# Kernel tuning notes

Measured on AMD Instinct MI355X. Metric: run time of the kernel, lower is better.

Reference implementation:

```python
import jax, jax.numpy as jnp
import numpy as np
from jax import lax

DN = ('NDHWC', 'DHWIO', 'NDHWC')
SHAPE = (33, 33, 33)
B = 2
N = 40000
C = 64


def setup_inputs() -> dict:
    key = jax.random.key(0)
    ks = jax.random.split(key, 24)
    D, H, W = SHAPE
    # unique active voxel coords (batch, z, y, x)
    rng = np.random.default_rng(0)
    idx = rng.choice(B * D * H * W, size=N, replace=False)
    b = idx // (D * H * W)
    r = idx % (D * H * W)
    coors = np.stack([b, r // (H * W), (r // W) % H, r % W], axis=1).astype(np.int32)

    def w(k, shape, scale=0.1):
        return jax.random.normal(k, shape, jnp.float32) * scale

    inp = {
        'features': jax.random.normal(ks[0], (N, 3), jnp.float32),
        'coors': jnp.asarray(coors),
        'batch_size': B,
        'w1': w(ks[1], (3, 3, 3, 3, C), 0.2), 'b1': w(ks[2], (C,), 0.05),
        'w2': w(ks[3], (3, 3, 3, C, C), 0.05), 'b2': w(ks[4], (C,), 0.05),
        'w3': w(ks[5], (3, 3, 3, C, C), 0.05), 'b3': w(ks[6], (C,), 0.05),
        'wt': w(ks[7], (3, 3, 3, C, C), 0.05), 'bt': w(ks[8], (C,), 0.05),
        'w5': w(ks[9], (3, 3, 3, C, C), 0.05), 'b5': w(ks[10], (C,), 0.05),
    }
    # folded eval-mode BatchNorm: y = x*s + h  (s = gamma/sqrt(var+eps), h = beta - mean*s)
    for i, (sk, hk) in enumerate(zip(ks[11:16], ks[16:21]), start=1):
        inp[f's{i}'] = 1.0 + 0.1 * jax.random.normal(sk, (C,), jnp.float32)
        inp[f'h{i}'] = 0.05 * jax.random.normal(hk, (C,), jnp.float32)
    return inp


def _forward(features, coors, batch_size,
             w1, b1, w2, b2, w3, b3, wt, bt, w5, b5,
             s1, h1, s2, h2, s3, h3, s4, h4, s5, h5):
    D, H, W = SHAPE
    bi, zi, yi, xi = coors[:, 0], coors[:, 1], coors[:, 2], coors[:, 3]
    # densify SparseConvTensor (zeros at inactive sites) + active mask
    x = jnp.zeros((batch_size, D, H, W, features.shape[-1]), features.dtype)
    x = x.at[bi, zi, yi, xi].set(features)
    m = jnp.zeros((batch_size, D, H, W, 1), jnp.float32).at[bi, zi, yi, xi].set(1.0)
    ones3 = jnp.ones((3, 3, 3, 1, 1), jnp.float32)

    conv = lambda a, k, pad: lax.conv_general_dilated(a, k, (1, 1, 1), pad, dimension_numbers=DN)
    # masked BN(eval) + ReLU: applied only on active sites, background stays exactly 0
    act = lambda y, mm, s, h: jnp.where(mm, jax.nn.relu(y * s + h), 0.0)

    # SparseConv3d(3,64,3): valid conv; output actives = 1-dilation of input actives
    x = conv(x, w1, 'VALID')
    m1 = conv(m, ones3, 'VALID') > 0  # [B,31,31,31,1]
    x = act(x + b1, m1, s1, h1)

    # two SubMConv3d(64,64,3) sharing indice_key: same active set, SAME padding
    x = act(conv(x, w2, 'SAME') + b2, m1, s2, h2)
    x = act(conv(x, w3, 'SAME') + b3, m1, s3, h3)

    # SparseConvTranspose3d(64,64,3,2): out = (D-1)*2+3; actives = transposed dilation
    x = lax.conv_transpose(x, wt, (2, 2, 2), 'VALID', dimension_numbers=DN)
    mT = lax.conv_transpose(m1.astype(jnp.float32), ones3, (2, 2, 2), 'VALID', dimension_numbers=DN) > 0
    x = act(x + bt, mT, s4, h4)

    # ToDense -> dense Conv3d(64,64,3) -> BN -> ReLU (dense: applied everywhere)
    x = conv(x, w5, 'VALID') + b5
    x = jax.nn.relu(x * s5 + h5)
    return jnp.transpose(x, (0, 4, 1, 2, 3))  # NCDHW like spconv ToDense output


def reference(features, coors, batch_size,
              w1, b1, w2, b2, w3, b3, wt, bt, w5, b5,
              s1, h1, s2, h2, s3, h3, s4, h4, s5, h5):
    return _forward(features, coors, batch_size,
                    w1, b1, w2, b2, w3, b3, wt, bt, w5, b5,
                    s1, h1, s2, h2, s3, h3, s4, h4, s5, h5)
```

## Files before the change

kernel.cpp:

```cpp
#include <hip/hip_runtime.h>
#include <cstdint>

constexpr int BB = 2, C = 64;
constexpr int D1 = 31;
constexpr int DP = 33;
constexpr int D4 = 63;
constexpr int D5 = 61;
constexpr int D5CUBE = D5*D5*D5;

constexpr int NV1 = BB*D1*D1*D1;
constexpr int NVP = BB*DP*DP*DP;
constexpr int NV4 = BB*D4*D4*D4;
constexpr int NV5 = BB*D5*D5*D5;

constexpr size_t alup(size_t x) { return (x + 255) & ~(size_t)255; }
constexpr size_t OB_X0  = 0;
constexpr size_t OB_M0  = alup(OB_X0  + (size_t)NVP*3*4);
constexpr size_t OB_M1P = alup(OB_M0  + (size_t)NVP*4);
constexpr size_t OB_X1  = alup(OB_M1P + (size_t)NVP*4);
constexpr size_t OB_X2  = alup(OB_X1  + (size_t)NVP*64*2);
constexpr size_t OB_X3  = alup(OB_X2  + (size_t)NVP*64*2);
constexpr size_t OB_MT  = alup(OB_X3  + (size_t)NVP*64*2);
constexpr size_t OB_X4  = alup(OB_MT  + (size_t)NV4*4);
constexpr size_t OB_WB2 = alup(OB_X4  + (size_t)NV4*64*2);
constexpr size_t OB_WB3 = alup(OB_WB2 + (size_t)27*64*64*2);
constexpr size_t OB_WBT = alup(OB_WB3 + (size_t)27*64*64*2);
constexpr size_t OB_WB5 = alup(OB_WBT + (size_t)27*64*64*2);

typedef __attribute__((ext_vector_type(8))) short short8;
typedef __attribute__((ext_vector_type(4))) float f32x4;

__device__ inline unsigned short f2bf(float f) {
  unsigned int u = __float_as_uint(f);
  u = (u + 0x7FFFu + ((u >> 16) & 1u)) >> 16;
  return (unsigned short)u;
}

template<int DD>
__device__ inline void decodev(int vox, int& b, int& z, int& y, int& x) {
  x = vox % DD; int r = vox / DD;
  y = r % DD;   r /= DD;
  z = r % DD;   b = r / DD;
}

__device__ inline int xcd_swz(int bid, int nb) {
  int q = nb >> 3, r = nb & 7;
  int xcd = bid & 7, idx = bid >> 3;
  return (xcd < r ? xcd*(q+1) : r*(q+1) + (xcd - r)*q) + idx;
}

__global__ void __launch_bounds__(256)
k_zero(float* __restrict__ x0, float* __restrict__ m0, float* __restrict__ m1p,
       unsigned short* __restrict__ x1, unsigned short* __restrict__ x2,
       unsigned short* __restrict__ x3) {
  int v = blockIdx.x*256 + threadIdx.x;
  if (v >= NVP) return;
  m0[v] = 0.f; m1p[v] = 0.f;
  x0[3*v+0] = 0.f; x0[3*v+1] = 0.f; x0[3*v+2] = 0.f;
  int x = v % DP, r = v / DP;
  int y = r % DP; r /= DP;
  int z = r % DP;
  if (x==0 || x==DP-1 || y==0 || y==DP-1 || z==0 || z==DP-1) {
    ulonglong2 zz = {0ull, 0ull};
    ulonglong2* p1 = (ulonglong2*)(x1 + (size_t)v*64);
    ulonglong2* p2 = (ulonglong2*)(x2 + (size_t)v*64);
    ulonglong2* p3 = (ulonglong2*)(x3 + (size_t)v*64);
    #pragma unroll
    for (int i = 0; i < 8; i++) { p1[i] = zz; p2[i] = zz; p3[i] = zz; }
  }
}

__global__ void k_scatter(const float* __restrict__ feat, const int* __restrict__ coors,
                          int n, float* __restrict__ x0, float* __restrict__ m0) {
  int i = blockIdx.x*blockDim.x + threadIdx.x;
  if (i >= n) return;
  int b = coors[4*i+0], z = coors[4*i+1], y = coors[4*i+2], x = coors[4*i+3];
  int v = ((b*DP + z)*DP + y)*DP + x;
  x0[v*3+0] = feat[3*i+0];
  x0[v*3+1] = feat[3*i+1];
  x0[v*3+2] = feat[3*i+2];
  m0[v] = 1.0f;
}

__global__ void __launch_bounds__(256)
k_conv1(const float* __restrict__ x0, const float* __restrict__ m0,
        unsigned short* __restrict__ x1, float* __restrict__ m1p,
        const float* __restrict__ w1, const float* __restrict__ b1,
        const float* __restrict__ s1, const float* __restrict__ h1) {
  long long t = (long long)blockIdx.x*blockDim.x + threadIdx.x;
  if (t >= (long long)NV1*C) return;
  int co  = (int)(t & 63);
  int vox = (int)(t >> 6);
  int b, z, y, x; decodev<D1>(vox, b, z, y, x);
  float sum = 0.f, mm = 0.f;
  #pragma unroll
  for (int kz=0; kz<3; kz++)
  #pragma unroll
  for (int ky=0; ky<3; ky++)
  #pragma unroll
  for (int kx=0; kx<3; kx++) {
    int iv = ((b*DP + z+kz)*DP + y+ky)*DP + (x+kx);
    mm += m0[iv];
    const float* px = x0 + iv*3;
    const float* pw = w1 + ((kz*3+ky)*3+kx)*3*64 + co;
    sum += px[0]*pw[0] + px[1]*pw[64] + px[2]*pw[128];
  }
  bool m = mm > 0.f;
  float o = m ? fmaxf((sum + b1[co])*s1[co] + h1[co], 0.f) : 0.f;
  size_t pOff = (size_t)(((b*DP + z+1)*DP + y+1)*DP + (x+1));
  x1[pOff*C + co] = f2bf(o);
  if (co == 0) m1p[pOff] = m ? 1.f : 0.f;
}

__global__ void k_repack4(const float* __restrict__ wa, const float* __restrict__ wb,
                          const float* __restrict__ wc, const float* __restrict__ wd,
                          unsigned short* __restrict__ da, unsigned short* __restrict__ db,
                          unsigned short* __restrict__ dc, unsigned short* __restrict__ dd) {
  int which = blockIdx.x / 432;
  int i = (blockIdx.x - which*432)*256 + threadIdx.x;
  const float* w = which == 0 ? wa : which == 1 ? wb : which == 2 ? wc : wd;
  unsigned short* dst = which == 0 ? da : which == 1 ? db : which == 2 ? dc : dd;
  int co = i & 63, k = (i >> 6) & 63, t = i >> 12;
  int kk = k >> 5, q = (k >> 3) & 3, j = k & 7, cb = co >> 4, l = q*16 + (co & 15);
  dst[(size_t)((t*2+kk)*4+cb)*512 + l*8 + j] = f2bf(w[i]);
}

template<int NA, int DOUT, int DIN>
__global__ void __launch_bounds__(256)
k_conv_mfma(const unsigned short* __restrict__ inBF, const unsigned short* __restrict__ wB,
            unsigned short* __restrict__ outPtr, const float* __restrict__ m1p,
            const float* __restrict__ bias, const float* __restrict__ s,
            const float* __restrict__ h) {
  constexpr int NVOX = BB*DOUT*DOUT*DOUT;
  const int lane = threadIdx.x & 63;
  const int wid  = threadIdx.x >> 6;
  const int wave = xcd_swz(blockIdx.x, gridDim.x)*4 + wid;
  const int vb   = wave * (NA*16);

  int rowb[NA];
  #pragma unroll
  for (int a = 0; a < NA; a++) {
    int vox = vb + a*16 + (lane & 15);
    vox = vox < NVOX ? vox : NVOX-1;
    int b, z, y, x; decodev<DOUT>(vox, b, z, y, x);
    rowb[a] = (((b*DIN + z)*DIN + y)*DIN + x)*64;
  }
  const int koff = (lane >> 4) * 8;

  f32x4 acc[NA][4];
  #pragma unroll
  for (int a = 0; a < NA; a++)
    #pragma unroll
    for (int cb = 0; cb < 4; cb++)
      acc[a][cb] = f32x4{0.f, 0.f, 0.f, 0.f};

  #pragma unroll 1
  for (int t = 0; t < 27; ++t) {
    int kz = t / 9, rr = t - kz*9;
    int ky = rr / 3, kx = rr - ky*3;
    const int toff = ((kz*DIN + ky)*DIN + kx)*64;
    #pragma unroll
    for (int kk = 0; kk < 2; ++kk) {
      short8 A[NA];
      #pragma unroll
      for (int a = 0; a < NA; a++)
        A[a] = *reinterpret_cast<const short8*>(inBF + rowb[a] + toff + kk*32 + koff);
      short8 Bv[4];
      const unsigned short* wp = wB + (size_t)(t*2+kk)*2048 + lane*8;
      #pragma unroll
      for (int cb = 0; cb < 4; cb++)
        Bv[cb] = *reinterpret_cast<const short8*>(wp + cb*512);
      #pragma unroll
      for (int a = 0; a < NA; a++)
        #pragma unroll
        for (int cb = 0; cb < 4; cb++)
          acc[a][cb] = __builtin_amdgcn_mfma_f32_16x16x32_bf16(A[a], Bv[cb], acc[a][cb], 0, 0, 0);
    }
  }

  float bv[4], sv[4], hv[4];
  #pragma unroll
  for (int cb = 0; cb < 4; cb++) {
    int c = cb*16 + (lane & 15);
    bv[cb] = bias[c]; sv[cb] = s[c]; hv[cb] = h[c];
  }

  #pragma unroll
  for (int a = 0; a < NA; a++)
    #pragma unroll
    for (int r = 0; r < 4; r++) {
      int vox = vb + a*16 + (lane >> 4)*4 + r;
      if (vox >= NVOX) continue;
      int b, z, y, x; decodev<DOUT>(vox, b, z, y, x);
      size_t pOff = (size_t)(((b*DP + z+1)*DP + y+1)*DP + (x+1));
      bool m = m1p[pOff] > 0.f;
      #pragma unroll
      for (int cb = 0; cb < 4; cb++) {
        float o = m ? fmaxf((acc[a][cb][r] + bv[cb])*sv[cb] + hv[cb], 0.f) : 0.f;
        outPtr[pOff*64 + cb*16 + (lane & 15)] = f2bf(o);
      }
    }
}

__global__ void __launch_bounds__(256)
k_maskT(const float* __restrict__ m1p, float* __restrict__ mt) {
  int vox = blockIdx.x*256 + threadIdx.x;
  if (vox >= NV4) return;
  int b, zo, yo, xo; decodev<D4>(vox, b, zo, yo, xo);
  float mm = 0.f;
  for (int kz = 0; kz < 3; kz++) {
    if ((zo + kz) & 1) continue;
    int izp = ((zo + kz - 2) >> 1) + 1;
    for (int ky = 0; ky < 3; ky++) {
      if ((yo + ky) & 1) continue;
      int iyp = ((yo + ky - 2) >> 1) + 1;
      for (int kx = 0; kx < 3; kx++) {
        if ((xo + kx) & 1) continue;
        int ixp = ((xo + kx - 2) >> 1) + 1;
        mm += m1p[((b*DP + izp)*DP + iyp)*DP + ixp];
      }
    }
  }
  mt[vox] = mm;
}

__global__ void __launch_bounds__(256)
k_convT_mfma(const unsigned short* __restrict__ x3, const unsigned short* __restrict__ wB,
             unsigned short* __restrict__ x4, const float* __restrict__ mt,
             const float* __restrict__ bias, const float* __restrict__ s,
             const float* __restrict__ h) {
  const int lane = threadIdx.x & 63;
  const int wid  = threadIdx.x >> 6;
  const int w    = xcd_swz(blockIdx.x, gridDim.x)*4 + wid;
  if (w >= BB*D4*D4) return;
  const int b  = w / (D4*D4);
  const int rm = w % (D4*D4);
  const int zo = rm / D4;
  const int yo = rm % D4;
  const int ii = lane & 15;
  const int koff = (lane >> 4) * 8;

  f32x4 acc[4][4];
  #pragma unroll
  for (int a = 0; a < 4; a++)
    #pragma unroll
    for (int cb = 0; cb < 4; cb++)
      acc[a][cb] = f32x4{0.f, 0.f, 0.f, 0.f};

  #pragma unroll 1
  for (int kz = 0; kz < 3; kz++) {
    if ((zo + kz) & 1) continue;
    const int izp = ((zo + kz - 2) >> 1) + 1;
    #pragma unroll 1
    for (int ky = 0; ky < 3; ky++) {
      if ((yo + ky) & 1) continue;
      const int iyp = ((yo + ky - 2) >> 1) + 1;
      const size_t planeBase = ((size_t)((b*DP + izp)*DP + iyp))*DP*64;
      #pragma unroll
      for (int kx = 0; kx < 3; kx++) {
        const int apar  = kx & 1;
        const int xoffE = ((kx + apar - 2) >> 1) + 1;
        const int t = (kz*3 + ky)*3 + kx;
        #pragma unroll
        for (int kk = 0; kk < 2; ++kk) {
          short8 Bv[4];
          const unsigned short* wpk = wB + (size_t)(t*2+kk)*2048 + lane*8;
          #pragma unroll
          for (int cb = 0; cb < 4; cb++)
            Bv[cb] = *reinterpret_cast<const short8*>(wpk + cb*512);
          #pragma unroll
          for (int ablk = 0; ablk < 2; ablk++) {
            const int ixp = ablk*16 + ii + xoffE;
            short8 A = *reinterpret_cast<const short8*>(x3 + planeBase + (size_t)ixp*64 + kk*32 + koff);
            const int afr = apar*2 + ablk;
            #pragma unroll
            for (int cb = 0; cb < 4; cb++)
              acc[afr][cb] = __builtin_amdgcn_mfma_f32_16x16x32_bf16(A, Bv[cb], acc[afr][cb], 0, 0, 0);
          }
        }
      }
    }
  }

  float bv[4], sv[4], hv[4];
  #pragma unroll
  for (int cb = 0; cb < 4; cb++) {
    int c = cb*16 + (lane & 15);
    bv[cb] = bias[c]; sv[cb] = s[c]; hv[cb] = h[c];
  }
  const int rowBase = ((b*D4 + zo)*D4 + yo)*D4;
  #pragma unroll
  for (int a = 0; a < 4; a++) {
    const int ablk = a & 1, apar = a >> 1;
    #pragma unroll
    for (int r = 0; r < 4; r++) {
      const int row = (lane >> 4)*4 + r;
      const int xo  = 2*(ablk*16 + row) + apar;
      if (xo >= D4) continue;
      const int vox = rowBase + xo;
      const bool m = mt[vox] > 0.f;
      #pragma unroll
      for (int cb = 0; cb < 4; cb++) {
        float o = m ? fmaxf((acc[a][cb][r] + bv[cb])*sv[cb] + hv[cb], 0.f) : 0.f;
        x4[(size_t)vox*64 + cb*16 + (lane & 15)] = f2bf(o);
      }
    }
  }
}

__device__ __forceinline__ void c5_step(const short8 (&A)[4], const short8 (&W)[4],
                                        f32x4 (&acc)[4][4]) {
  #pragma unroll
  for (int a = 0; a < 4; a++)
    #pragma unroll
    for (int cb = 0; cb < 4; cb++)
      acc[a][cb] = __builtin_amdgcn_mfma_f32_16x16x32_bf16(W[cb], A[a], acc[a][cb], 0, 0, 0);
}

__global__ void __launch_bounds__(256, 2)
k_conv5_mfma(const unsigned short* __restrict__ x4, const unsigned short* __restrict__ wB,
             float* __restrict__ out, const float* __restrict__ bias,
             const float* __restrict__ s, const float* __restrict__ h) {
  __shared__ short8 sA[2][2048];
  const int tid  = threadIdx.x;
  const int lane = tid & 63;
  const int wid  = tid >> 6;
  const int ll   = lane & 15;
  const int l16  = lane >> 4;

  const int blk   = xcd_swz(blockIdx.x, gridDim.x);
  const int ytile = blk & 15;
  const int rzb   = blk >> 4;
  const int z     = rzb % D5;
  const int b     = rzb / D5;
  const int y0    = ytile * 4;

  int st_r[8], st_base[8];
  #pragma unroll
  for (int it = 0; it < 8; ++it) {
    int g = it*256 + tid; g = g > 2015 ? 2015 : g;
    int r = g / 504, rem = g - r*504;
    int v = rem >> 3, c16p = rem & 7;
    int c16l = c16p ^ (v & 7);
    st_r[it] = r;
    st_base[it] = (v << 7) + (c16l << 4);
  }

  const char* x4b = (const char*)x4;

  f32x4 acc[4][4];
  #pragma unroll
  for (int a = 0; a < 4; a++)
    #pragma unroll
    for (int cb = 0; cb < 4; cb++)
      acc[a][cb] = f32x4{0.f, 0.f, 0.f, 0.f};

  auto STAGE_A = [&](int kzn, int kyn, int hn) {
    size_t pb = (size_t)(b*D4 + z + kzn) * (D4*D4*128);
    char* dst = (char*)&sA[hn][0];
    #pragma unroll
    for (int it = 0; it < 8; ++it) {
      int yin = y0 + st_r[it] + kyn; yin = yin > 62 ? 62 : yin;
      __builtin_amdgcn_global_load_lds(
        (const __attribute__((address_space(1))) void*)(x4b + pb + (size_t)yin*8064 + st_base[it]),
        (__attribute__((address_space(3))) void*)(dst + it*4096 + wid*1024),
        16, 0, 0);
    }
  };
  auto LDA = [&](int hh, int kx, int kk, short8 (&A)[4]) {
    #pragma unroll
    for (int a = 0; a < 4; a++) {
      int v  = a*16 + ll + kx;
      int ch = wid*504 + v*8 + ((kk*4 + l16) ^ (v & 7));
      A[a] = sA[hh][ch];
    }
  };

  short8 A0[4], A1[4], A2[4];

  STAGE_A(0, 0, 0);
  __syncthreads();

#define C5_BODY(p0,p1,p2,p3,p4,p5)                                    \
  do {                                                                 \
    LDA(hh, (p0)>>1, (p0)&1, A0);                                      \
    LDA(hh, (p1)>>1, (p1)&1, A1);                                      \
    LDA(hh, (p2)>>1, (p2)&1, A2);  c5_step(A0, W[p0], acc);            \
    LDA(hh, (p3)>>1, (p3)&1, A0);  c5_step(A1, W[p1], acc);            \
    LDA(hh, (p4)>>1, (p4)&1, A1);  c5_step(A2, W[p2], acc);            \
    LDA(hh, (p5)>>1, (p5)&1, A2);  c5_step(A0, W[p3], acc);            \
    c5_step(A1, W[p4], acc);                                           \
    c5_step(A2, W[p5], acc);                                           \
  } while (0)

  int kzn = 0, kyn = 1;
  #pragma unroll 1
  for (int p = 0; p < 9; ++p) {
    const int hh = p & 1;

    short8 W[6][4];
    {
      const unsigned short* wp = wB + (size_t)p*12288 + lane*8;
      #pragma unroll
      for (int st = 0; st < 6; ++st)
        #pragma unroll
        for (int cb = 0; cb < 4; cb++)
          W[st][cb] = *reinterpret_cast<const short8*>(wp + st*2048 + cb*512);
    }
    __builtin_amdgcn_sched_barrier(0);

    if (p < 8) {
      STAGE_A(kzn, kyn, hh ^ 1);
      kyn++; if (kyn == 3) { kyn = 0; kzn++; }
    }
    __builtin_amdgcn_sched_barrier(0);

    if ((wid & 1) == 0) {
      C5_BODY(0,1,2,3,4,5);
    } else {
      C5_BODY(3,4,5,0,1,2);
    }
    __syncthreads();
  }
#undef C5_BODY

  const int yout = y0 + wid;
  if (yout < D5) {
    #pragma unroll
    for (int a = 0; a < 4; a++) {
      int x = a*16 + ll;
      if (x >= D5) continue;
      size_t sp = (size_t)(z*D5 + yout)*D5 + x;
      #pragma unroll
      for (int cb = 0; cb < 4; cb++)
        #pragma unroll
        for (int r = 0; r < 4; r++) {
          int co = cb*16 + l16*4 + r;
          float o = fmaxf((acc[a][cb][r] + bias[co])*s[co] + h[co], 0.f);
          out[(size_t)(b*64 + co)*D5CUBE + sp] = o;
        }
    }
  }
}

extern "C" void kernel_launch(void* const* d_in, const int* in_sizes, int n_in,
                              void* d_out, int out_size, void* d_ws, size_t ws_size,
                              hipStream_t stream) {
  const float* feat  = (const float*)d_in[0];
  const int*   coors = (const int*)d_in[1];
  const float* w1 = (const float*)d_in[3];
  const float* b1 = (const float*)d_in[4];
  const float* w2 = (const float*)d_in[5];
  const float* b2 = (const float*)d_in[6];
  const float* w3 = (const float*)d_in[7];
  const float* b3 = (const float*)d_in[8];
  const float* wt = (const float*)d_in[9];
  const float* bt = (const float*)d_in[10];
  const float* w5 = (const float*)d_in[11];
  const float* b5 = (const float*)d_in[12];
  const float* s1 = (const float*)d_in[13];
  const float* h1 = (const float*)d_in[14];
  const float* s2 = (const float*)d_in[15];
  const float* h2 = (const float*)d_in[16];
  const float* s3 = (const float*)d_in[17];
  const float* h3 = (const float*)d_in[18];
  const float* s4 = (const float*)d_in[19];
  const float* h4 = (const float*)d_in[20];
  const float* s5 = (const float*)d_in[21];
  const float* h5 = (const float*)d_in[22];
  int n = in_sizes[0] / 3;

  char* wsb = (char*)d_ws;
  float*          X0  = (float*)(wsb + OB_X0);
  float*          M0  = (float*)(wsb + OB_M0);
  float*          M1P = (float*)(wsb + OB_M1P);
  unsigned short* X1  = (unsigned short*)(wsb + OB_X1);
  unsigned short* X2  = (unsigned short*)(wsb + OB_X2);
  unsigned short* X3  = (unsigned short*)(wsb + OB_X3);
  float*          MT  = (float*)(wsb + OB_MT);
  unsigned short* X4  = (unsigned short*)(wsb + OB_X4);
  unsigned short* WB2 = (unsigned short*)(wsb + OB_WB2);
  unsigned short* WB3 = (unsigned short*)(wsb + OB_WB3);
  unsigned short* WBT = (unsigned short*)(wsb + OB_WBT);
  unsigned short* WB5 = (unsigned short*)(wsb + OB_WB5);

  k_zero<<<(NVP + 255)/256, 256, 0, stream>>>(X0, M0, M1P, X1, X2, X3);

  k_repack4<<<1728, 256, 0, stream>>>(w2, w3, wt, w5, WB2, WB3, WBT, WB5);

  k_scatter<<<(n+255)/256, 256, 0, stream>>>(feat, coors, n, X0, M0);

  {
    long long threads = (long long)NV1*C;
    k_conv1<<<(int)((threads+255)/256), 256, 0, stream>>>(X0, M0, X1, M1P, w1, b1, s1, h1);
  }

  constexpr int WAVES23 = (NV1 + 31) / 32;
  constexpr int BLK23   = (WAVES23 + 3) / 4;
  k_conv_mfma<2, D1, DP><<<BLK23, 256, 0, stream>>>(X1, WB2, X2, M1P, b2, s2, h2);
  k_conv_mfma<2, D1, DP><<<BLK23, 256, 0, stream>>>(X2, WB3, X3, M1P, b3, s3, h3);

  k_maskT<<<(NV4 + 255)/256, 256, 0, stream>>>(M1P, MT);

  constexpr int ROWS_T = BB*D4*D4;
  k_convT_mfma<<<(ROWS_T + 3)/4, 256, 0, stream>>>(X3, WBT, X4, MT, bt, s4, h4);

  constexpr int BLK5 = BB * D5 * 16;
  k_conv5_mfma<<<BLK5, 256, 0, stream>>>(X4, WB5, (float*)d_out, b5, s5, h5);
}
```

Measured before the change: 366.2 us.

## Stage transposed-conv input planes in LDS shared across four output rows

The transposed convolution kernel now has each block handle four consecutive y output rows at one z. The input rows they need (up to 2 z planes × 3 y rows × 33 voxels × 64 channels) are loaded once into an XOR-swizzled LDS buffer with global_load_lds, and waves read A fragments from LDS instead of global memory. This removes repeated global/L2 reads of the same input rows by neighbouring output rows. In exchange it adds about 28KB of LDS per block and a block-wide barrier before compute, and waves whose row falls past the edge sit idle.

```diff
diff --git a/kernel.cpp b/kernel.cpp
--- a/kernel.cpp
+++ b/kernel.cpp
@@ -224,21 +224,47 @@
   mt[vox] = mm;
 }
 
+constexpr int CT_CHUNKS = 1792;
+
 __global__ void __launch_bounds__(256)
 k_convT_mfma(const unsigned short* __restrict__ x3, const unsigned short* __restrict__ wB,
              unsigned short* __restrict__ x4, const float* __restrict__ mt,
              const float* __restrict__ bias, const float* __restrict__ s,
              const float* __restrict__ h) {
-  const int lane = threadIdx.x & 63;
-  const int wid  = threadIdx.x >> 6;
-  const int w    = xcd_swz(blockIdx.x, gridDim.x)*4 + wid;
-  if (w >= BB*D4*D4) return;
-  const int b  = w / (D4*D4);
-  const int rm = w % (D4*D4);
-  const int zo = rm / D4;
-  const int yo = rm % D4;
-  const int ii = lane & 15;
-  const int koff = (lane >> 4) * 8;
+  __shared__ short8 sb[CT_CHUNKS];
+  const int tid  = threadIdx.x;
+  const int lane = tid & 63;
+  const int wid  = tid >> 6;
+  const int ii   = lane & 15;
+  const int l16  = lane >> 4;
+
+  const int blk   = xcd_swz(blockIdx.x, gridDim.x);
+  const int ytile = blk & 15;
+  const int rzb   = blk >> 4;
+  const int zo    = rzb % D4;
+  const int b     = rzb / D4;
+  const int y0    = ytile * 4;
+
+  const int izp0 = (zo + (zo & 1)) >> 1;
+  const int izp1 = (zo & 1) ? izp0 : izp0 + 1;
+
+  #pragma unroll
+  for (int it = 0; it < 7; ++it) {
+    int g = it*256 + tid; g = g > 1583 ? 1583 : g;
+    int r6 = g / 264, rem = g - r6*264;
+    int v = rem >> 3, c16p = rem & 7;
+    int c16l = c16p ^ (v & 7);
+    int pz  = r6 >= 3 ? 1 : 0;
+    int ry  = r6 - pz*3;
+    int izp = pz ? izp1 : izp0;
+    int iyp = ytile*2 + ry;
+    size_t srcB = ((size_t)((b*DP + izp)*DP + iyp)*DP)*128 + (size_t)(v << 7) + (c16l << 4);
+    __builtin_amdgcn_global_load_lds(
+      (const __attribute__((address_space(1))) void*)((const char*)x3 + srcB),
+      (__attribute__((address_space(3))) void*)((char*)&sb[0] + it*4096 + wid*1024),
+      16, 0, 0);
+  }
+  __syncthreads();
 
   f32x4 acc[4][4];
   #pragma unroll
@@ -247,62 +273,67 @@
     for (int cb = 0; cb < 4; cb++)
       acc[a][cb] = f32x4{0.f, 0.f, 0.f, 0.f};
 
-  #pragma unroll 1
-  for (int kz = 0; kz < 3; kz++) {
-    if ((zo + kz) & 1) continue;
-    const int izp = ((zo + kz - 2) >> 1) + 1;
+  const int yo = y0 + wid;
+  if (yo < D4) {
+    const int nPz = (zo & 1) ? 1 : 2;
     #pragma unroll 1
-    for (int ky = 0; ky < 3; ky++) {
-      if ((yo + ky) & 1) continue;
-      const int iyp = ((yo + ky - 2) >> 1) + 1;
-      const size_t planeBase = ((size_t)((b*DP + izp)*DP + iyp))*DP*64;
-      #pragma unroll
-      for (int kx = 0; kx < 3; kx++) {
-        const int apar  = kx & 1;
-        const int xoffE = ((kx + apar - 2) >> 1) + 1;
-        const int t = (kz*3 + ky)*3 + kx;
+    for (int pz = 0; pz < 2; ++pz) {
+      if (pz >= nPz) break;
+      const int kz = (zo & 1) ? 1 : pz*2;
+      #pragma unroll 1
+      for (int kyi = 0; kyi < 2; ++kyi) {
+        int ky, ry;
+        if (wid & 1) { if (kyi == 1) break; ky = 1; ry = (wid + 1) >> 1; }
+        else         { ky = kyi*2;          ry = (wid >> 1) + kyi; }
+        const int rbase = (pz*3 + ry)*264;
         #pragma unroll
-        for (int kk = 0; kk < 2; ++kk) {
-          short8 Bv[4];
-          const unsigned short* wpk = wB + (size_t)(t*2+kk)*2048 + lane*8;
+        for (int kx = 0; kx < 3; ++kx) {
+          const int apar  = kx & 1;
+          const int xoffE = ((kx + apar - 2) >> 1) + 1;
+          const int t = (kz*3 + ky)*3 + kx;
           #pragma unroll
-          for (int cb = 0; cb < 4; cb++)
-            Bv[cb] = *reinterpret_cast<const short8*>(wpk + cb*512);
-          #pragma unroll
-          for (int ablk = 0; ablk < 2; ablk++) {
-            const int ixp = ablk*16 + ii + xoffE;
-            short8 A = *reinterpret_cast<const short8*>(x3 + planeBase + (size_t)ixp*64 + kk*32 + koff);
-            const int afr = apar*2 + ablk;
+          for (int kk = 0; kk < 2; ++kk) {
+            short8 Bv[4];
+            const unsigned short* wpk = wB + (size_t)(t*2+kk)*2048 + lane*8;
             #pragma unroll
             for (int cb = 0; cb < 4; cb++)
-              acc[afr][cb] = __builtin_amdgcn_mfma_f32_16x16x32_bf16(A, Bv[cb], acc[afr][cb], 0, 0, 0);
+              Bv[cb] = *reinterpret_cast<const short8*>(wpk + cb*512);
+            #pragma unroll
+            for (int ablk = 0; ablk < 2; ablk++) {
+              const int ixp = ablk*16 + ii + xoffE;
+              short8 A = sb[rbase + ixp*8 + ((kk*4 + l16) ^ (ixp & 7))];
+              const int afr = apar*2 + ablk;
+              #pragma unroll
+              for (int cb = 0; cb < 4; cb++)
+                acc[afr][cb] = __builtin_amdgcn_mfma_f32_16x16x32_bf16(A, Bv[cb], acc[afr][cb], 0, 0, 0);
+            }
           }
         }
       }
     }
-  }
-
-  float bv[4], sv[4], hv[4];
-  #pragma unroll
-  for (int cb = 0; cb < 4; cb++) {
-    int c = cb*16 + (lane & 15);
-    bv[cb] = bias[c]; sv[cb] = s[c]; hv[cb] = h[c];
-  }
-  const int rowBase = ((b*D4 + zo)*D4 + yo)*D4;
-  #pragma unroll
-  for (int a = 0; a < 4; a++) {
-    const int ablk = a & 1, apar = a >> 1;
-    #pragma unroll
-    for (int r = 0; r < 4; r++) {
-      const int row = (lane >> 4)*4 + r;
-      const int xo  = 2*(ablk*16 + row) + apar;
-      if (xo >= D4) continue;
-      const int vox = rowBase + xo;
-      const bool m = mt[vox] > 0.f;
-      #pragma unroll
-      for (int cb = 0; cb < 4; cb++) {
-        float o = m ? fmaxf((acc[a][cb][r] + bv[cb])*sv[cb] + hv[cb], 0.f) : 0.f;
-        x4[(size_t)vox*64 + cb*16 + (lane & 15)] = f2bf(o);
+
+    float bv[4], sv[4], hv[4];
+    #pragma unroll
+    for (int cb = 0; cb < 4; cb++) {
+      int c = cb*16 + (lane & 15);
+      bv[cb] = bias[c]; sv[cb] = s[c]; hv[cb] = h[c];
+    }
+    const int rowBase = ((b*D4 + zo)*D4 + yo)*D4;
+    #pragma unroll
+    for (int a = 0; a < 4; a++) {
+      const int ablk = a & 1, apar = a >> 1;
+      #pragma unroll
+      for (int r = 0; r < 4; r++) {
+        const int row = (lane >> 4)*4 + r;
+        const int xo  = 2*(ablk*16 + row) + apar;
+        if (xo >= D4) continue;
+        const int vox = rowBase + xo;
+        const bool m = mt[vox] > 0.f;
+        #pragma unroll
+        for (int cb = 0; cb < 4; cb++) {
+          float o = m ? fmaxf((acc[a][cb][r] + bv[cb])*sv[cb] + hv[cb], 0.f) : 0.f;
+          x4[(size_t)vox*64 + cb*16 + (lane & 15)] = f2bf(o);
+        }
       }
     }
   }
@@ -502,8 +533,8 @@
 
   k_maskT<<<(NV4 + 255)/256, 256, 0, stream>>>(M1P, MT);
 
-  constexpr int ROWS_T = BB*D4*D4;
-  k_convT_mfma<<<(ROWS_T + 3)/4, 256, 0, stream>>>(X3, WBT, X4, MT, bt, s4, h4);
+  constexpr int BLK_T = BB * D4 * 16;
+  k_convT_mfma<<<BLK_T, 256, 0, stream>>>(X3, WBT, X4, MT, bt, s4, h4);
 
   constexpr int BLK5 = BB * D5 * 16;
   k_conv5_mfma<<<BLK5, 256, 0, stream>>>(X4, WB5, (float*)d_out, b5, s5, h5);
```

Result: faster. 349.3 us (-4.6%).
